# Optimization experiments

Measured on AMD Instinct MI355X. Metric: run time of the kernel, lower is better.

The kernel has to match this reference:

```python
import jax, jax.numpy as jnp
import numpy as np

C_M, C_Z, H, C = 256, 128, 8, 32  # msa emb, pair emb, heads, head channels
S, R = 128, 256                   # MSA rows, residues


def layer_norm(x, gamma, beta, eps=1e-5):
    mu = jnp.mean(x, axis=-1, keepdims=True)
    var = jnp.var(x, axis=-1, keepdims=True)
    return (x - mu) * jax.lax.rsqrt(var + eps) * gamma + beta


def setup_inputs() -> dict:
    key = jax.random.key(0)
    ks = jax.random.split(key, 12)
    sc_m = 1.0 / np.sqrt(C_M)
    sc_z = 1.0 / np.sqrt(C_Z)
    sc_hc = 1.0 / np.sqrt(H * C)
    return {
        "msa_rep": jax.random.normal(ks[0], (S, R, C_M), dtype=jnp.float32),
        "pair_rep": jax.random.normal(ks[1], (R, R, C_Z), dtype=jnp.float32),
        "ln_msa_g": jnp.ones((C_M,), jnp.float32),
        "ln_msa_b": jnp.zeros((C_M,), jnp.float32),
        "ln_pair_g": jnp.ones((C_Z,), jnp.float32),
        "ln_pair_b": jnp.zeros((C_Z,), jnp.float32),
        "w_q": jax.random.normal(ks[2], (C_M, H, C), jnp.float32) * sc_m,
        "w_k": jax.random.normal(ks[3], (C_M, H, C), jnp.float32) * sc_m,
        "w_v": jax.random.normal(ks[4], (C_M, H, C), jnp.float32) * sc_m,
        "w_g": jax.random.normal(ks[5], (C_M, H, C), jnp.float32) * sc_m,
        "b_g": jnp.zeros((H, C), jnp.float32),
        "w_b": jax.random.normal(ks[6], (C_Z, H), jnp.float32) * sc_z,
        "b_b": jnp.zeros((H,), jnp.float32),
        "w_o": jax.random.normal(ks[7], (H, C, C_M), jnp.float32) * sc_hc,
        "b_o": jnp.zeros((C_M,), jnp.float32),
    }


def reference(msa_rep, pair_rep, ln_msa_g, ln_msa_b, ln_pair_g, ln_pair_b,
              w_q, w_k, w_v, w_g, b_g, w_b, b_b, w_o, b_o):
    m = layer_norm(msa_rep, ln_msa_g, ln_msa_b)                 # [S,R,C_M]
    q = jnp.einsum('src,chd->srhd', m, w_q)                     # [S,R,H,C]
    k = jnp.einsum('src,chd->srhd', m, w_k)
    v = jnp.einsum('src,chd->srhd', m, w_v)
    gates = jax.nn.sigmoid(jnp.einsum('src,chd->srhd', m, w_g) + b_g)
    # pair bias: [R,R,H] -> [H,R,R]
    z = layer_norm(pair_rep, ln_pair_g, ln_pair_b)
    b = jnp.einsum('ijc,ch->hij', z, w_b) + b_b[:, None, None]  # [H,R,R]
    logits = jnp.einsum('sqhd,skhd->shqk', q, k) / np.sqrt(C)   # [S,H,R,R]
    logits = logits + b[None]
    w = jax.nn.softmax(logits, axis=-1)
    o = jnp.einsum('shqk,skhd->sqhd', w, v)                     # [S,R,H,C]
    o = gates * o
    out = jnp.einsum('srhd,hdc->src', o, w_o) + b_o             # [S,R,C_M]
    return out
```

## Files before the change

### kernel.cpp

```cpp
#include <hip/hip_runtime.h>
#include <hip/hip_bf16.h>

#define S_DIM 128
#define R_DIM 256
#define CM 256
#define CZ 128
#define H_DIM 8
#define C_DIM 32

typedef short bf16x8 __attribute__((ext_vector_type(8)));
typedef float f32x4 __attribute__((ext_vector_type(4)));

__device__ inline ushort f2b(float f) {
  __hip_bfloat16 b = __float2bfloat16(f);
  return *(ushort*)&b;
}
__device__ inline float b2f(ushort u) {
  __hip_bfloat16 b = *(__hip_bfloat16*)&u;
  return __bfloat162float(b);
}

__device__ __forceinline__ void gld_lds16(const ushort* g, ushort* l) {
  __builtin_amdgcn_global_load_lds(
      (const __attribute__((address_space(1))) unsigned int*)g,
      (__attribute__((address_space(3))) unsigned int*)l, 16, 0, 0);
}

__global__ __launch_bounds__(256) void wt_kernel(
    const float* __restrict__ wq, const float* __restrict__ wk,
    const float* __restrict__ wv, const float* __restrict__ wg,
    const float* __restrict__ wo, ushort* __restrict__ Wt5) {
  __shared__ float t[64][65];
  int z = blockIdx.z;
  const float* W = (z == 0) ? wq : (z == 1) ? wk : (z == 2) ? wv
                   : (z == 3) ? wg : wo;
  ushort* Wt = Wt5 + (size_t)z * 65536;
  int tid = threadIdx.x;
  int r = tid >> 2, c4 = (tid & 3) * 16;
  int rowBase = blockIdx.y * 64, colBase = blockIdx.x * 64;
#pragma unroll
  for (int j = 0; j < 16; ++j)
    t[r][c4 + j] = W[(size_t)(rowBase + r) * 256 + colBase + c4 + j];
  __syncthreads();
#pragma unroll
  for (int j = 0; j < 16; ++j)
    Wt[(size_t)(colBase + r) * 256 + rowBase + c4 + j] = f2b(t[c4 + j][r]);
}

__global__ __launch_bounds__(256) void ln_msa_kernel(
    const float* __restrict__ x, const float* __restrict__ g,
    const float* __restrict__ b, ushort* __restrict__ m) {
  int lane = threadIdx.x & 63, w = threadIdx.x >> 6;
  int row = blockIdx.x * 4 + w;
  const float* xp = x + (size_t)row * CM + lane * 4;
  float4 v = *(const float4*)xp;
  float s1 = v.x + v.y + v.z + v.w;
  float s2 = v.x * v.x + v.y * v.y + v.z * v.z + v.w * v.w;
#pragma unroll
  for (int off = 32; off; off >>= 1) {
    s1 += __shfl_xor(s1, off, 64);
    s2 += __shfl_xor(s2, off, 64);
  }
  float mean = s1 * (1.0f / CM);
  float rstd = rsqrtf(s2 * (1.0f / CM) - mean * mean + 1e-5f);
  float4 gv = *(const float4*)(g + lane * 4);
  float4 bv = *(const float4*)(b + lane * 4);
  ushort4 o;
  o.x = f2b((v.x - mean) * rstd * gv.x + bv.x);
  o.y = f2b((v.y - mean) * rstd * gv.y + bv.y);
  o.z = f2b((v.z - mean) * rstd * gv.z + bv.z);
  o.w = f2b((v.w - mean) * rstd * gv.w + bv.w);
  *(ushort4*)(m + (size_t)row * CM + lane * 4) = o;
}

__global__ __launch_bounds__(256) void pair_bias_kernel(
    const float* __restrict__ z, const float* __restrict__ g,
    const float* __restrict__ b, const float* __restrict__ w_b,
    const float* __restrict__ b_b, float* __restrict__ bias) {
  __shared__ float wbs[CZ][8];
  __shared__ float gs[CZ], bs[CZ];
  int tid = threadIdx.x;
  if (tid < CZ) { gs[tid] = g[tid]; bs[tid] = b[tid]; }
  for (int i = tid; i < CZ * 8; i += 256) wbs[i >> 3][i & 7] = w_b[i];
  __syncthreads();
  int q = tid & 3;
  int row = blockIdx.x * 64 + (tid >> 2);
  const float* zp = z + (size_t)row * CZ + q * 32;
  float4 v[8];
#pragma unroll
  for (int j = 0; j < 8; ++j) v[j] = *(const float4*)(zp + j * 4);
  float s1 = 0.f, s2 = 0.f;
#pragma unroll
  for (int j = 0; j < 8; ++j) {
    s1 += v[j].x + v[j].y + v[j].z + v[j].w;
    s2 += v[j].x * v[j].x + v[j].y * v[j].y + v[j].z * v[j].z +
          v[j].w * v[j].w;
  }
  s1 += __shfl_xor(s1, 1, 64);
  s2 += __shfl_xor(s2, 1, 64);
  s1 += __shfl_xor(s1, 2, 64);
  s2 += __shfl_xor(s2, 2, 64);
  float mean = s1 * (1.0f / CZ);
  float var = s2 * (1.0f / CZ) - mean * mean;
  float rstd = rsqrtf(var + 1e-5f);
  float acc[8] = {};
#pragma unroll
  for (int j = 0; j < 8; ++j) {
    float e[4] = {v[j].x, v[j].y, v[j].z, v[j].w};
#pragma unroll
    for (int u = 0; u < 4; ++u) {
      int c = q * 32 + j * 4 + u;
      float zn = (e[u] - mean) * rstd * gs[c] + bs[c];
#pragma unroll
      for (int h = 0; h < 8; ++h) acc[h] += zn * wbs[c][h];
    }
  }
#pragma unroll
  for (int h = 0; h < 8; ++h) {
    acc[h] += __shfl_xor(acc[h], 1, 64);
    acc[h] += __shfl_xor(acc[h], 2, 64);
  }
  int h0 = q * 2;
  bias[(size_t)h0 * (R_DIM * R_DIM) + row] = acc[h0] + b_b[h0];
  bias[(size_t)(h0 + 1) * (R_DIM * R_DIM) + row] = acc[h0 + 1] + b_b[h0 + 1];
}

__global__ __launch_bounds__(256) void proj_mfma(
    const ushort* __restrict__ M, const ushort* __restrict__ Wt5,
    const float* __restrict__ b_g, ushort* __restrict__ qb,
    ushort* __restrict__ kb2, ushort* __restrict__ vb,
    ushort* __restrict__ gb) {
  __shared__ ushort As[128 * 64];
  __shared__ ushort Bs[64 * 64];
  int tid = threadIdx.x, lane = tid & 63, wid = tid >> 6;
  int lr = lane & 15, lg = lane >> 4;
  int rowBase = blockIdx.x * 128;
  int cby = blockIdx.y;
  int proj = cby >> 2;
  int sc = (lane & 7) ^ ((lane >> 3) & 7);
  const ushort* Ag =
      M + (size_t)(rowBase + wid * 32 + (lane >> 3)) * 256 + sc * 8;
  const ushort* Bg =
      Wt5 + (size_t)(cby * 64 + wid * 16 + (lane >> 3)) * 256 + sc * 8;
  ushort* Asl = As + wid * (32 * 64);
  ushort* Bsl = Bs + wid * (16 * 64);
  int wr = wid >> 1, wc = wid & 1;
  int sx = (lr & 7) * 8;
  f32x4 zf = {0.f, 0.f, 0.f, 0.f};
  f32x4 acc[4][2];
#pragma unroll
  for (int i = 0; i < 4; ++i)
#pragma unroll
    for (int j = 0; j < 2; ++j) acc[i][j] = zf;

  for (int kb = 0; kb < 4; ++kb) {
    if (kb) __syncthreads();
#pragma unroll
    for (int c = 0; c < 4; ++c)
      gld_lds16(Ag + kb * 64 + c * (8 * 256), Asl + c * (8 * 64));
#pragma unroll
    for (int c = 0; c < 2; ++c)
      gld_lds16(Bg + kb * 64 + c * (8 * 256), Bsl + c * (8 * 64));
    __syncthreads();
#pragma unroll
    for (int kk = 0; kk < 2; ++kk) {
      bf16x8 a[4], b[2];
#pragma unroll
      for (int mf = 0; mf < 4; ++mf)
        a[mf] = *(const bf16x8*)&As[(wr * 64 + mf * 16 + lr) * 64 +
                                    ((kk * 32 + lg * 8) ^ sx)];
#pragma unroll
      for (int nf = 0; nf < 2; ++nf)
        b[nf] = *(const bf16x8*)&Bs[(wc * 32 + nf * 16 + lr) * 64 +
                                    ((kk * 32 + lg * 8) ^ sx)];
#pragma unroll
      for (int mf = 0; mf < 4; ++mf)
#pragma unroll
        for (int nf = 0; nf < 2; ++nf)
          acc[mf][nf] = __builtin_amdgcn_mfma_f32_16x16x32_bf16(
              b[nf], a[mf], acc[mf][nf], 0, 0, 0);
    }
  }
#pragma unroll
  for (int mf = 0; mf < 4; ++mf) {
    int row = rowBase + wr * 64 + mf * 16 + lr;
    int s = row >> 8, rr = row & 255;
#pragma unroll
    for (int nf = 0; nf < 2; ++nf) {
      int colL = (cby & 3) * 64 + wc * 32 + nf * 16 + lg * 4;
      int h = colL >> 5, d0 = colL & 31;
      size_t oidx = ((size_t)((s * H_DIM + h) * R_DIM + rr)) * C_DIM + d0;
      f32x4 v4 = acc[mf][nf];
      ushort4 o4;
      if (proj == 0) {
        o4.x = f2b(v4[0] * 0.17677669529663687f);
        o4.y = f2b(v4[1] * 0.17677669529663687f);
        o4.z = f2b(v4[2] * 0.17677669529663687f);
        o4.w = f2b(v4[3] * 0.17677669529663687f);
        *(ushort4*)(qb + oidx) = o4;
      } else if (proj == 1) {
        o4.x = f2b(v4[0]); o4.y = f2b(v4[1]);
        o4.z = f2b(v4[2]); o4.w = f2b(v4[3]);
        *(ushort4*)(kb2 + oidx) = o4;
      } else if (proj == 2) {
        o4.x = f2b(v4[0]); o4.y = f2b(v4[1]);
        o4.z = f2b(v4[2]); o4.w = f2b(v4[3]);
        *(ushort4*)(vb + oidx) = o4;
      } else {
        float4 bg4 = *(const float4*)(b_g + colL);
        o4.x = f2b(1.f / (1.f + __expf(-(v4[0] + bg4.x))));
        o4.y = f2b(1.f / (1.f + __expf(-(v4[1] + bg4.y))));
        o4.z = f2b(1.f / (1.f + __expf(-(v4[2] + bg4.z))));
        o4.w = f2b(1.f / (1.f + __expf(-(v4[3] + bg4.w))));
        *(ushort4*)(gb + oidx) = o4;
      }
    }
  }
}

__global__ __launch_bounds__(512, 4) void attn_mfma(
    const ushort* __restrict__ q, const ushort* __restrict__ k,
    const ushort* __restrict__ v, const ushort* __restrict__ g,
    const float* __restrict__ bias, ushort* __restrict__ ob) {
  __shared__ ushort Vt[32][264];
  __shared__ ushort Pl[8][32][72];
  int blk = blockIdx.x;
  int s = blk >> 3, h = blk & 7;
  int tid = threadIdx.x, lane = tid & 63, w = tid >> 6;
  int lr = lane & 15, lg = lane >> 4;
  size_t base = (size_t)(s * H_DIM + h) * (R_DIM * C_DIM);

  {
    int key = tid >> 1, half = (tid & 1) * 16;
    const ushort* vp = v + base + (size_t)key * 32 + half;
    bf16x8 t0 = *(const bf16x8*)vp;
    bf16x8 t1 = *(const bf16x8*)(vp + 8);
#pragma unroll
    for (int j = 0; j < 8; ++j) {
      Vt[half + j][key] = (ushort)t0[j];
      Vt[half + 8 + j][key] = (ushort)t1[j];
    }
  }
  __syncthreads();

  int qrow0 = w * 32;
  bf16x8 qf[2];
#pragma unroll
  for (int mf = 0; mf < 2; ++mf)
    qf[mf] = *(const bf16x8*)(q + base + (size_t)(qrow0 + mf * 16 + lr) * 32 +
                              lg * 8);
  const float* bp0 = bias + ((size_t)h * R_DIM + qrow0 + lg * 4) * R_DIM +
                     lr * 4;

  float lsum[2][4] = {};
  f32x4 of[2][2];
  f32x4 zf = {0.f, 0.f, 0.f, 0.f};
#pragma unroll
  for (int mf = 0; mf < 2; ++mf) {
    of[mf][0] = zf;
    of[mf][1] = zf;
  }

  for (int t = 0; t < 4; ++t) {
    int k0 = t * 64;
    bf16x8 kf[4];
#pragma unroll
    for (int nf = 0; nf < 4; ++nf)
      kf[nf] = *(const bf16x8*)(k + base + (size_t)(k0 + lr * 4 + nf) * 32 +
                                lg * 8);
    f32x4 sf[2][4];
#pragma unroll
    for (int mf = 0; mf < 2; ++mf)
#pragma unroll
      for (int nf = 0; nf < 4; ++nf)
        sf[mf][nf] =
            __builtin_amdgcn_mfma_f32_16x16x32_bf16(qf[mf], kf[nf], zf, 0, 0, 0);
#pragma unroll
    for (int mf = 0; mf < 2; ++mf) {
      float4 bv[4];
#pragma unroll
      for (int r = 0; r < 4; ++r)
        bv[r] = *(const float4*)(bp0 + (size_t)(mf * 16 + r) * R_DIM + k0);
#pragma unroll
      for (int r = 0; r < 4; ++r) {
        float p0 = __expf(sf[mf][0][r] + bv[r].x);
        float p1 = __expf(sf[mf][1][r] + bv[r].y);
        float p2 = __expf(sf[mf][2][r] + bv[r].z);
        float p3 = __expf(sf[mf][3][r] + bv[r].w);
        lsum[mf][r] += (p0 + p1) + (p2 + p3);
        ushort4 pk;
        pk.x = f2b(p0);
        pk.y = f2b(p1);
        pk.z = f2b(p2);
        pk.w = f2b(p3);
        *(ushort4*)&Pl[w][mf * 16 + lg * 4 + r][lr * 4] = pk;
      }
    }
#pragma unroll
    for (int kt = 0; kt < 2; ++kt) {
      bf16x8 pf[2], vf[2];
#pragma unroll
      for (int mf = 0; mf < 2; ++mf)
        pf[mf] = *(const bf16x8*)&Pl[w][mf * 16 + lr][kt * 32 + lg * 8];
#pragma unroll
      for (int df = 0; df < 2; ++df)
        vf[df] = *(const bf16x8*)&Vt[df * 16 + lr][k0 + kt * 32 + lg * 8];
#pragma unroll
      for (int mf = 0; mf < 2; ++mf)
#pragma unroll
        for (int df = 0; df < 2; ++df)
          of[mf][df] = __builtin_amdgcn_mfma_f32_16x16x32_bf16(
              vf[df], pf[mf], of[mf][df], 0, 0, 0);
    }
  }
#pragma unroll
  for (int mf = 0; mf < 2; ++mf)
#pragma unroll
    for (int r = 0; r < 4; ++r) {
#pragma unroll
      for (int msk = 1; msk <= 8; msk <<= 1)
        lsum[mf][r] += __shfl_xor(lsum[mf][r], msk, 64);
    }
  int srcl = ((lr >> 2) << 4) + lr;
  float invr[2];
#pragma unroll
  for (int mf = 0; mf < 2; ++mf) {
    float t0 = __shfl(lsum[mf][0], srcl, 64);
    float t1 = __shfl(lsum[mf][1], srcl, 64);
    float t2 = __shfl(lsum[mf][2], srcl, 64);
    float t3 = __shfl(lsum[mf][3], srcl, 64);
    int rb = lr & 3;
    float lv = rb == 0 ? t0 : rb == 1 ? t1 : rb == 2 ? t2 : t3;
    invr[mf] = 1.f / lv;
  }
#pragma unroll
  for (int mf = 0; mf < 2; ++mf) {
    int row = qrow0 + mf * 16 + lr;
#pragma unroll
    for (int df = 0; df < 2; ++df) {
      int d0 = df * 16 + lg * 4;
      ushort4 g4 = *(const ushort4*)(g + base + (size_t)row * 32 + d0);
      ushort4 o4;
      o4.x = f2b(of[mf][df][0] * invr[mf] * b2f(g4.x));
      o4.y = f2b(of[mf][df][1] * invr[mf] * b2f(g4.y));
      o4.z = f2b(of[mf][df][2] * invr[mf] * b2f(g4.z));
      o4.w = f2b(of[mf][df][3] * invr[mf] * b2f(g4.w));
      *(ushort4*)(ob + ((size_t)(s * R_DIM + row)) * 256 + h * 32 + d0) = o4;
    }
  }
}

__global__ __launch_bounds__(256) void out_mfma(
    const ushort* __restrict__ A, const ushort* __restrict__ Wt,
    const float* __restrict__ b_o, float* __restrict__ out) {
  __shared__ ushort As[128 * 64];
  __shared__ ushort Bs[64 * 64];
  int tid = threadIdx.x, lane = tid & 63, wid = tid >> 6;
  int lr = lane & 15, lg = lane >> 4;
  int rowBase = blockIdx.x * 128;
  int colBase = blockIdx.y * 64;
  int sc = (lane & 7) ^ ((lane >> 3) & 7);
  const ushort* Ag =
      A + (size_t)(rowBase + wid * 32 + (lane >> 3)) * 256 + sc * 8;
  const ushort* Bg =
      Wt + (size_t)(colBase + wid * 16 + (lane >> 3)) * 256 + sc * 8;
  ushort* Asl = As + wid * (32 * 64);
  ushort* Bsl = Bs + wid * (16 * 64);
  int wr = wid >> 1, wc = wid & 1;
  int sx = (lr & 7) * 8;
  f32x4 zf = {0.f, 0.f, 0.f, 0.f};
  f32x4 acc[4][2];
#pragma unroll
  for (int i = 0; i < 4; ++i)
#pragma unroll
    for (int j = 0; j < 2; ++j) acc[i][j] = zf;

  for (int kb = 0; kb < 4; ++kb) {
    if (kb) __syncthreads();
#pragma unroll
    for (int c = 0; c < 4; ++c)
      gld_lds16(Ag + kb * 64 + c * (8 * 256), Asl + c * (8 * 64));
#pragma unroll
    for (int c = 0; c < 2; ++c)
      gld_lds16(Bg + kb * 64 + c * (8 * 256), Bsl + c * (8 * 64));
    __syncthreads();
#pragma unroll
    for (int kk = 0; kk < 2; ++kk) {
      bf16x8 a[4], b[2];
#pragma unroll
      for (int mf = 0; mf < 4; ++mf)
        a[mf] = *(const bf16x8*)&As[(wr * 64 + mf * 16 + lr) * 64 +
                                    ((kk * 32 + lg * 8) ^ sx)];
#pragma unroll
      for (int nf = 0; nf < 2; ++nf)
        b[nf] = *(const bf16x8*)&Bs[(wc * 32 + nf * 16 + lr) * 64 +
                                    ((kk * 32 + lg * 8) ^ sx)];
#pragma unroll
      for (int mf = 0; mf < 4; ++mf)
#pragma unroll
        for (int nf = 0; nf < 2; ++nf)
          acc[mf][nf] = __builtin_amdgcn_mfma_f32_16x16x32_bf16(
              b[nf], a[mf], acc[mf][nf], 0, 0, 0);
    }
  }
#pragma unroll
  for (int mf = 0; mf < 4; ++mf) {
    int row = rowBase + wr * 64 + mf * 16 + lr;
#pragma unroll
    for (int nf = 0; nf < 2; ++nf) {
      int col0 = colBase + wc * 32 + nf * 16 + lg * 4;
      float4 bo4 = *(const float4*)(b_o + col0);
      float4 o4;
      o4.x = acc[mf][nf][0] + bo4.x;
      o4.y = acc[mf][nf][1] + bo4.y;
      o4.z = acc[mf][nf][2] + bo4.z;
      o4.w = acc[mf][nf][3] + bo4.w;
      *(float4*)(out + (size_t)row * 256 + col0) = o4;
    }
  }
}

extern "C" void kernel_launch(void* const* d_in, const int* in_sizes, int n_in,
                              void* d_out, int out_size, void* d_ws,
                              size_t ws_size, hipStream_t stream) {
  const float* msa      = (const float*)d_in[0];
  const float* pair     = (const float*)d_in[1];
  const float* ln_msa_g = (const float*)d_in[2];
  const float* ln_msa_b = (const float*)d_in[3];
  const float* ln_pr_g  = (const float*)d_in[4];
  const float* ln_pr_b  = (const float*)d_in[5];
  const float* w_q      = (const float*)d_in[6];
  const float* w_k      = (const float*)d_in[7];
  const float* w_v      = (const float*)d_in[8];
  const float* w_g      = (const float*)d_in[9];
  const float* b_g      = (const float*)d_in[10];
  const float* w_b      = (const float*)d_in[11];
  const float* b_b      = (const float*)d_in[12];
  const float* w_o      = (const float*)d_in[13];
  const float* b_o      = (const float*)d_in[14];
  float* out = (float*)d_out;

  char* ws = (char*)d_ws;
  ushort* m   = (ushort*)(ws + 0);
  ushort* qb  = (ushort*)(ws + 16777216ull);
  ushort* kb  = (ushort*)(ws + 33554432ull);
  ushort* vb  = (ushort*)(ws + 50331648ull);
  ushort* gb  = (ushort*)(ws + 67108864ull);
  float*  bi  = (float*) (ws + 83886080ull);
  ushort* ob  = (ushort*)(ws + 85983232ull);
  ushort* Wt5 = (ushort*)(ws + 102760448ull);

  wt_kernel<<<dim3(4, 4, 5), 256, 0, stream>>>(w_q, w_k, w_v, w_g, w_o, Wt5);
  ln_msa_kernel<<<S_DIM * R_DIM / 4, 256, 0, stream>>>(msa, ln_msa_g,
                                                       ln_msa_b, m);
  pair_bias_kernel<<<R_DIM * R_DIM / 64, 256, 0, stream>>>(
      pair, ln_pr_g, ln_pr_b, w_b, b_b, bi);
  proj_mfma<<<dim3(256, 16), 256, 0, stream>>>(m, Wt5, b_g, qb, kb, vb, gb);
  attn_mfma<<<S_DIM * H_DIM, 512, 0, stream>>>(qb, kb, vb, gb, bi, ob);
  out_mfma<<<dim3(256, 4), 256, 0, stream>>>(ob, Wt5 + 4 * 65536, b_o, out);
}
```

Before: 119.0 us.

## Split attention tile loop per query fragment to cut registers and LDS

Restructures the attention inner loop so each 16-row query fragment does its scores, softmax exponentials, P store and PV MFMAs before the next fragment starts. This halves the per-wave P staging buffer and shrinks live score registers. The launch bound rises to 8 blocks per CU and the LDS row padding changes. The aim is higher occupancy, at the risk of register spills under the tighter bound. The new padded row strides (266 and 66 halfwords) also break 16-byte alignment for the vector LDS reads.

```diff
diff --git a/kernel.cpp b/kernel.cpp
--- a/kernel.cpp
+++ b/kernel.cpp
@@ -218,12 +218,12 @@
   }
 }
 
-__global__ __launch_bounds__(512, 4) void attn_mfma(
+__global__ __launch_bounds__(512, 8) void attn_mfma(
     const ushort* __restrict__ q, const ushort* __restrict__ k,
     const ushort* __restrict__ v, const ushort* __restrict__ g,
     const float* __restrict__ bias, ushort* __restrict__ ob) {
-  __shared__ ushort Vt[32][264];
-  __shared__ ushort Pl[8][32][72];
+  __shared__ ushort Vt[32][266];
+  __shared__ ushort Pl[8][16][66];
   int blk = blockIdx.x;
   int s = blk >> 3, h = blk & 7;
   int tid = threadIdx.x, lane = tid & 63, w = tid >> 6;
@@ -268,49 +268,41 @@
     for (int nf = 0; nf < 4; ++nf)
       kf[nf] = *(const bf16x8*)(k + base + (size_t)(k0 + lr * 4 + nf) * 32 +
                                 lg * 8);
-    f32x4 sf[2][4];
-#pragma unroll
-    for (int mf = 0; mf < 2; ++mf)
+#pragma unroll
+    for (int mf = 0; mf < 2; ++mf) {
+      f32x4 sf[4];
 #pragma unroll
       for (int nf = 0; nf < 4; ++nf)
-        sf[mf][nf] =
+        sf[nf] =
             __builtin_amdgcn_mfma_f32_16x16x32_bf16(qf[mf], kf[nf], zf, 0, 0, 0);
-#pragma unroll
-    for (int mf = 0; mf < 2; ++mf) {
       float4 bv[4];
 #pragma unroll
       for (int r = 0; r < 4; ++r)
         bv[r] = *(const float4*)(bp0 + (size_t)(mf * 16 + r) * R_DIM + k0);
 #pragma unroll
       for (int r = 0; r < 4; ++r) {
-        float p0 = __expf(sf[mf][0][r] + bv[r].x);
-        float p1 = __expf(sf[mf][1][r] + bv[r].y);
-        float p2 = __expf(sf[mf][2][r] + bv[r].z);
-        float p3 = __expf(sf[mf][3][r] + bv[r].w);
+        float p0 = __expf(sf[0][r] + bv[r].x);
+        float p1 = __expf(sf[1][r] + bv[r].y);
+        float p2 = __expf(sf[2][r] + bv[r].z);
+        float p3 = __expf(sf[3][r] + bv[r].w);
         lsum[mf][r] += (p0 + p1) + (p2 + p3);
         ushort4 pk;
         pk.x = f2b(p0);
         pk.y = f2b(p1);
         pk.z = f2b(p2);
         pk.w = f2b(p3);
-        *(ushort4*)&Pl[w][mf * 16 + lg * 4 + r][lr * 4] = pk;
+        *(ushort4*)&Pl[w][lg * 4 + r][lr * 4] = pk;
       }
-    }
-#pragma unroll
-    for (int kt = 0; kt < 2; ++kt) {
-      bf16x8 pf[2], vf[2];
-#pragma unroll
-      for (int mf = 0; mf < 2; ++mf)
-        pf[mf] = *(const bf16x8*)&Pl[w][mf * 16 + lr][kt * 32 + lg * 8];
-#pragma unroll
-      for (int df = 0; df < 2; ++df)
-        vf[df] = *(const bf16x8*)&Vt[df * 16 + lr][k0 + kt * 32 + lg * 8];
-#pragma unroll
-      for (int mf = 0; mf < 2; ++mf)
-#pragma unroll
-        for (int df = 0; df < 2; ++df)
-          of[mf][df] = __builtin_amdgcn_mfma_f32_16x16x32_bf16(
-              vf[df], pf[mf], of[mf][df], 0, 0, 0);
+#pragma unroll
+      for (int kt = 0; kt < 2; ++kt) {
+        bf16x8 pf = *(const bf16x8*)&Pl[w][lr][kt * 32 + lg * 8];
+        bf16x8 vf0 = *(const bf16x8*)&Vt[lr][k0 + kt * 32 + lg * 8];
+        bf16x8 vf1 = *(const bf16x8*)&Vt[16 + lr][k0 + kt * 32 + lg * 8];
+        of[mf][0] = __builtin_amdgcn_mfma_f32_16x16x32_bf16(
+            vf0, pf, of[mf][0], 0, 0, 0);
+        of[mf][1] = __builtin_amdgcn_mfma_f32_16x16x32_bf16(
+            vf1, pf, of[mf][1], 0, 0, 0);
+      }
     }
   }
 #pragma unroll
```

After: 171.4 us. 1.44x slower.
